# Optimization experiments

Measured on AMD Instinct MI355X. Metric: run time of the kernel, lower is better.

## Reference

```python
import jax, jax.numpy as jnp
import numpy as np

B = 2048
DIMS = [300, 74, 35]
R = 3
ENC = 150
HID = 32
CAT = ENC * R  # 450


def setup_inputs() -> dict:
    key = jax.random.key(0)
    ks = jax.random.split(key, 32)
    d = {}
    for i, dim in enumerate(DIMS):
        d[f"x{i}"] = jax.random.normal(ks[i], (B, 1, dim), dtype=jnp.float32)
    s = 0.05
    for i, dim in enumerate(DIMS):
        d[f"encW{i}"] = jax.random.normal(ks[3 + 2 * i], (ENC, dim), dtype=jnp.float32) * s
        d[f"encb{i}"] = jax.random.normal(ks[4 + 2 * i], (ENC,), dtype=jnp.float32) * s
    d["affw"] = jax.random.normal(ks[10], (R,), dtype=jnp.float32) * s      # Linear(1,1) weight per branch
    d["Ww"] = jax.random.normal(ks[11], (R, HID, 1), dtype=jnp.float32) * s  # Linear(1,32)
    d["Wc"] = jax.random.normal(ks[12], (R, HID, CAT), dtype=jnp.float32) * s  # Linear(450,32)
    d["Wh"] = jax.random.normal(ks[13], (R, 1, HID), dtype=jnp.float32) * s   # Linear(32,1)
    d["clsW1"] = jax.random.normal(ks[14], (128, CAT), dtype=jnp.float32) * s
    d["clsb1"] = jax.random.normal(ks[15], (128,), dtype=jnp.float32) * s
    d["clsW2"] = jax.random.normal(ks[16], (7, 128), dtype=jnp.float32) * s
    d["clsb2"] = jax.random.normal(ks[17], (7,), dtype=jnp.float32) * s
    return d


def reference(x0, x1, x2, encW0, encb0, encW1, encb1, encW2, encb2,
              affw, Ww, Wc, Wh, clsW1, clsb1, clsW2, clsb2):
    xs = [x0, x1, x2]
    encW = [encW0, encW1, encW2]
    encb = [encb0, encb1, encb2]
    # Encode each modality: [B,1,dim_i] -> [B,1,150]
    enc = [jnp.einsum('btd,ed->bte', xs[i], encW[i]) + encb[i] for i in range(R)]
    feat_n = jnp.concatenate(enc, axis=2)            # [B,1,450]
    scale = 1.0 / jnp.sqrt(jnp.float32(feat_n.shape[1]))  # T=1
    att_feats = []
    for i in range(R):
        enc_t = jnp.swapaxes(enc[i], 1, 2)           # [B,150,1]
        t = jnp.swapaxes(feat_n, 1, 2) * affw[i]     # [B,450,1] (Linear(1,1), no bias)
        # outer product attention: [B,150,1] @ [B,1,450] -> [B,150,450]
        att = jnp.tanh(jnp.matmul(enc_t, jnp.swapaxes(t, 1, 2)) * scale)
        a = jnp.einsum('bec,hc->beh', att, Wc[i])    # [B,150,32]
        b = jnp.matmul(enc_t, Ww[i].T)               # [B,150,1]@[1,32] -> [B,150,32]
        H = jax.nn.relu(a + b)
        out_i = jnp.swapaxes(jnp.matmul(H, Wh[i].T), 1, 2) + enc[i]  # [B,1,150]
        att_feats.append(out_i)
    feats = jnp.concatenate(att_feats, axis=2)       # [B,1,450]
    # classifier (dropout is identity in eval mode)
    h = jnp.einsum('btc,kc->btk', feats, clsW1) + clsb1
    return jnp.einsum('btk,ok->bto', h, clsW2) + clsb2
```

## Files before the change

### kernel.cpp

```cpp
#include <hip/hip_runtime.h>
#include <math.h>

#define NJ 4
#define DEG 7
#define X0f 1.1f
#define NB 8
#define NT 768

struct Poly { float c[NJ]; };

typedef float v4f __attribute__((ext_vector_type(4)));

__global__ __launch_bounds__(256) void k_repack(
    const float* __restrict__ Wc, const float* __restrict__ W1,
    const float* __restrict__ eW0, const float* __restrict__ eW1, const float* __restrict__ eW2,
    float* __restrict__ WcT, float* __restrict__ W1T,
    float* __restrict__ Wt0, float* __restrict__ Wt1, float* __restrict__ Wt2) {
    int tid = blockIdx.x * 256 + threadIdx.x;
    int stride = gridDim.x * 256;
    for (int idx = tid; idx < 3 * 464 * 32; idx += stride) {
        int i = idx / (464 * 32); int rem = idx - i * 464 * 32;
        int m = rem >> 5, h = rem & 31;
        float v = 0.f;
        if (m < 456) {
            int seg = m / 152, e = m - seg * 152;
            if (e < 150) v = Wc[((size_t)i * 32 + h) * 450 + seg * 150 + e];
        }
        WcT[idx] = v;
    }
    for (int idx = tid; idx < 456 * 128; idx += stride) {
        int m = idx >> 7, k = idx & 127;
        int seg = m / 152, e = m - seg * 152;
        W1T[idx] = (e < 150) ? W1[k * 450 + seg * 150 + e] : 0.f;
    }
    for (int idx = tid; idx < 304 * 152; idx += stride) {
        int d = idx / 152, e = idx - d * 152;
        Wt0[idx] = (d < 300 && e < 150) ? eW0[e * 300 + d] : 0.f;
    }
    for (int idx = tid; idx < 76 * 152; idx += stride) {
        int d = idx / 152, e = idx - d * 152;
        Wt1[idx] = (d < 74 && e < 150) ? eW1[e * 74 + d] : 0.f;
    }
    for (int idx = tid; idx < 36 * 152; idx += stride) {
        int d = idx / 152, e = idx - d * 152;
        Wt2[idx] = (d < 35 && e < 150) ? eW2[e * 35 + d] : 0.f;
    }
}

__global__ __launch_bounds__(NT, 1) void k_fused(
    const float* __restrict__ x0, const float* __restrict__ x1, const float* __restrict__ x2,
    const float* __restrict__ eb0, const float* __restrict__ eb1, const float* __restrict__ eb2,
    const float* __restrict__ Wt0, const float* __restrict__ Wt1, const float* __restrict__ Wt2,
    const float* __restrict__ WcT,
    const float* __restrict__ affw, const float* __restrict__ Ww, const float* __restrict__ Wh,
    const float* __restrict__ W1T, const float* __restrict__ cb1,
    const float* __restrict__ cW2, const float* __restrict__ cb2,
    float* __restrict__ out, Poly pc) {
#pragma clang fp contract(fast)
    __shared__ __align__(16) float xs[NB * 428];
    __shared__ __align__(16) float featf[NB * 468];
    __shared__ __align__(16) float fof[NB * 468];
    __shared__ __align__(16) float wWs[96], wHs[96];

    int tid = threadIdx.x;
    int b0 = blockIdx.x * NB;

    if (tid < 96) { wWs[tid] = Ww[tid]; wHs[tid] = Wh[tid]; }
    if (tid >= 96 && tid < 192) {
        int q = tid - 96; int b = q / 12, r = q - b * 12;
        featf[b * 468 + 456 + r] = 0.f;
    }
    if (tid >= 192 && tid < 240) {
        int q = tid - 192; int b = q / 6, r = q - b * 6;
        fof[b * 468 + (r >> 1) * 152 + 150 + (r & 1)] = 0.f;
    }
    for (int idx = tid; idx < NB * 75; idx += NT) {
        int b = idx / 75, q = idx - b * 75;
        ((v4f*)(xs + b * 428))[q] = ((const v4f*)(x0 + (size_t)(b0 + b) * 300))[q];
    }
    for (int idx = tid; idx < NB * 74; idx += NT) {
        int b = idx / 74, d = idx - b * 74;
        xs[b * 428 + 304 + d] = x1[(size_t)(b0 + b) * 74 + d];
    }
    for (int idx = tid; idx < NB * 35; idx += NT) {
        int b = idx / 35, d = idx - b * 35;
        xs[b * 428 + 380 + d] = x2[(size_t)(b0 + b) * 35 + d];
    }
    __syncthreads();

    {
        int tasks[2]; int nt = 1;
        tasks[0] = tid;
        if (tid >= 624) { tasks[nt++] = 768 + (767 - tid); }
        for (int q = 0; q < nt; ++q) {
            int task = tasks[q];
            int b = task & 7, m4 = task >> 3;
            int seg = (m4 >= 76) ? 2 : (m4 >= 38) ? 1 : 0;
            int e4 = m4 - seg * 38;
            const float* eb = seg == 0 ? eb0 : seg == 1 ? eb1 : eb2;
            const v4f* Wt4 = (const v4f*)(seg == 0 ? Wt0 : seg == 1 ? Wt1 : Wt2) + e4;
            const float* xb = xs + b * 428 + (seg == 0 ? 0 : seg == 1 ? 304 : 380);
            int DP4 = seg == 0 ? 76 : seg == 1 ? 19 : 9;
            const v4f* xr = (const v4f*)xb;
            int e = e4 * 4;
            v4f acc = { (e < 150) ? eb[e] : 0.f,
                        (e + 1 < 150) ? eb[e + 1] : 0.f,
                        (e + 2 < 150) ? eb[e + 2] : 0.f,
                        (e + 3 < 150) ? eb[e + 3] : 0.f };
            for (int d4 = 0; d4 < DP4; ++d4) {
                v4f x4 = xr[d4];
                v4f w0 = Wt4[(d4 * 4 + 0) * 38];
                v4f w1 = Wt4[(d4 * 4 + 1) * 38];
                v4f w2 = Wt4[(d4 * 4 + 2) * 38];
                v4f w3 = Wt4[(d4 * 4 + 3) * 38];
                acc += x4.x * w0;
                acc += x4.y * w1;
                acc += x4.z * w2;
                acc += x4.w * w3;
            }
            ((v4f*)(featf + b * 468))[m4] = acc;
        }
    }
    __syncthreads();

    {
        int w = tid >> 6;
        int i = w >> 2, wp = w & 3;
        int lane = tid & 63;
        int hq = lane & 7, slice = lane >> 3;
        int slice2 = (lane >> 3) & 3, bh = lane >> 5;
        float aff = affw[i];
        const v4f* Wb4 = (const v4f*)WcT + (size_t)i * 3712 + hq;
        int bA = wp * 2, bB = bA + 1;
        const v4f* frowA = (const v4f*)(featf + bA * 468);
        const v4f* frowB = (const v4f*)(featf + bB * 468);

        v4f accA[NJ], accB[NJ];
        #pragma unroll
        for (int J = 0; J < NJ; ++J) { accA[J] = (v4f)0.f; accB[J] = (v4f)0.f; }
        float mxA = 0.f, mxB = 0.f;

        int m4lo = (slice < 4) ? slice * 15 : 60 + (slice - 4) * 14;
        int m4n  = (slice < 4) ? 15 : 14;
        #pragma unroll 3
        for (int k = 0; k < m4n; ++k) {
            int m4 = m4lo + k;
            v4f fA = frowA[m4];
            v4f fB = frowB[m4];
            const v4f* wp4 = Wb4 + m4 * 32;
            v4f w0 = wp4[0];
            v4f w1 = wp4[8];
            v4f w2 = wp4[16];
            v4f w3 = wp4[24];
            mxA = fmaxf(mxA, fmaxf(fmaxf(fabsf(fA.x), fabsf(fA.y)), fmaxf(fabsf(fA.z), fabsf(fA.w))));
            mxB = fmaxf(mxB, fmaxf(fmaxf(fabsf(fB.x), fabsf(fB.y)), fmaxf(fabsf(fB.z), fabsf(fB.w))));
            {
                float g0 = aff * fA.x, g1 = aff * fA.y, g2 = aff * fA.z, g3 = aff * fA.w;
                float q0 = g0 * g0, q1 = g1 * g1, q2 = g2 * g2, q3 = g3 * g3;
                float p0 = g0, p1 = g1, p2 = g2, p3 = g3;
                accA[0] += p0 * w0; accA[0] += p1 * w1; accA[0] += p2 * w2; accA[0] += p3 * w3;
                #pragma unroll
                for (int J = 1; J < NJ; ++J) {
                    p0 *= q0; p1 *= q1; p2 *= q2; p3 *= q3;
                    accA[J] += p0 * w0; accA[J] += p1 * w1; accA[J] += p2 * w2; accA[J] += p3 * w3;
                }
            }
            {
                float g0 = aff * fB.x, g1 = aff * fB.y, g2 = aff * fB.z, g3 = aff * fB.w;
                float q0 = g0 * g0, q1 = g1 * g1, q2 = g2 * g2, q3 = g3 * g3;
                float p0 = g0, p1 = g1, p2 = g2, p3 = g3;
                accB[0] += p0 * w0; accB[0] += p1 * w1; accB[0] += p2 * w2; accB[0] += p3 * w3;
                #pragma unroll
                for (int J = 1; J < NJ; ++J) {
                    p0 *= q0; p1 *= q1; p2 *= q2; p3 *= q3;
                    accB[J] += p0 * w0; accB[J] += p1 * w1; accB[J] += p2 * w2; accB[J] += p3 * w3;
                }
            }
        }
        #pragma unroll
        for (int J = 0; J < NJ; ++J) {
            float cJ = pc.c[J];
            float vx, vy, vz, vw;
            vx = accA[J].x; vx += __shfl_xor(vx, 8); vx += __shfl_xor(vx, 16); vx += __shfl_xor(vx, 32);
            vy = accA[J].y; vy += __shfl_xor(vy, 8); vy += __shfl_xor(vy, 16); vy += __shfl_xor(vy, 32);
            vz = accA[J].z; vz += __shfl_xor(vz, 8); vz += __shfl_xor(vz, 16); vz += __shfl_xor(vz, 32);
            vw = accA[J].w; vw += __shfl_xor(vw, 8); vw += __shfl_xor(vw, 16); vw += __shfl_xor(vw, 32);
            accA[J] = (v4f){ vx * cJ, vy * cJ, vz * cJ, vw * cJ };
            vx = accB[J].x; vx += __shfl_xor(vx, 8); vx += __shfl_xor(vx, 16); vx += __shfl_xor(vx, 32);
            vy = accB[J].y; vy += __shfl_xor(vy, 8); vy += __shfl_xor(vy, 16); vy += __shfl_xor(vy, 32);
            vz = accB[J].z; vz += __shfl_xor(vz, 8); vz += __shfl_xor(vz, 16); vz += __shfl_xor(vz, 32);
            vw = accB[J].w; vw += __shfl_xor(vw, 8); vw += __shfl_xor(vw, 16); vw += __shfl_xor(vw, 32);
            accB[J] = (v4f){ vx * cJ, vy * cJ, vz * cJ, vw * cJ };
        }
        mxA = fmaxf(mxA, __shfl_xor(mxA, 8));
        mxA = fmaxf(mxA, __shfl_xor(mxA, 16));
        mxA = fmaxf(mxA, __shfl_xor(mxA, 32));
        mxB = fmaxf(mxB, __shfl_xor(mxB, 8));
        mxB = fmaxf(mxB, __shfl_xor(mxB, 16));
        mxB = fmaxf(mxB, __shfl_xor(mxB, 32));

        v4f Ms[NJ];
        #pragma unroll
        for (int J = 0; J < NJ; ++J) Ms[J] = bh ? accB[J] : accA[J];
        float gmax = fabsf(aff) * (bh ? mxB : mxA);
        int b = bA + bh;
        const float* fb = featf + b * 468;
        const v4f* frow = bh ? frowB : frowA;

        v4f wW4 = ((const v4f*)wWs)[i * 8 + hq];
        v4f wH4 = ((const v4f*)wHs)[i * 8 + hq];
        int e4lo = slice2 * 10;
        int e4hi = (slice2 == 3) ? 38 : (e4lo + 10);
        for (int e4 = e4lo; e4 < e4hi; ++e4) {
            v4f s4 = frow[i * 38 + e4];
            float ores[4];
            #pragma unroll
            for (int r = 0; r < 4; ++r) {
                float s = (r == 0) ? s4.x : (r == 1) ? s4.y : (r == 2) ? s4.z : s4.w;
                v4f a4;
                if (fabsf(s) * gmax <= X0f) {
                    float s2 = s * s, p = s;
                    a4 = Ms[0] * p;
                    #pragma unroll
                    for (int J = 1; J < NJ; ++J) { p *= s2; a4 += p * Ms[J]; }
                } else {
                    a4 = (v4f)0.f;
                    for (int c = 0; c < 456; ++c) {
                        float t = tanhf(s * aff * fb[c]);
                        a4 += t * Wb4[c * 8];
                    }
                }
                v4f hv = s * wW4 + a4;
                hv = __builtin_elementwise_max(hv, (v4f)0.f);
                v4f dv = hv * wH4;
                float csum = dv.x + dv.y + dv.z + dv.w;
                csum += __shfl_xor(csum, 1);
                csum += __shfl_xor(csum, 2);
                csum += __shfl_xor(csum, 4);
                ores[r] = csum + s;
            }
            if (hq == 0)
                ((v4f*)(fof + b * 468))[i * 38 + e4] = (v4f){ ores[0], ores[1], ores[2], ores[3] };
        }
    }
    __syncthreads();

    {
        int cs = tid >> 8;
        int rr = tid & 255;
        int b = rr & 7, k4 = rr >> 3;
        const v4f* W14 = (const v4f*)W1T + k4;
        const v4f* fr = (const v4f*)(fof + b * 468);
        v4f a = (v4f)0.f;
        int c4lo = cs * 38;
        for (int c4 = c4lo; c4 < c4lo + 38; ++c4) {
            v4f fv = fr[c4];
            v4f w0 = W14[(c4 * 4 + 0) * 32];
            v4f w1 = W14[(c4 * 4 + 1) * 32];
            v4f w2 = W14[(c4 * 4 + 2) * 32];
            v4f w3 = W14[(c4 * 4 + 3) * 32];
            a += fv.x * w0;
            a += fv.y * w1;
            a += fv.z * w2;
            a += fv.w * w3;
        }
        ((v4f*)xs)[(cs * 8 + b) * 33 + k4] = a;
    }
    __syncthreads();
    if (tid < 256) {
        int b = tid >> 5, k4 = tid & 31;
        const v4f* hp4 = (const v4f*)xs;
        v4f v  = hp4[(0 * 8 + b) * 33 + k4];
        v4f v1 = hp4[(1 * 8 + b) * 33 + k4];
        v4f v2 = hp4[(2 * 8 + b) * 33 + k4];
        v4f bias = ((const v4f*)cb1)[k4];
        v = v + v1 + v2 + bias;
        ((v4f*)(featf + b * 468))[k4] = v;
    }
    __syncthreads();
    if (tid < NB * 7) {
        int b = tid / 7, o = tid - (tid / 7) * 7;
        const v4f* hb = (const v4f*)(featf + b * 468);
        const v4f* w2 = (const v4f*)(cW2 + o * 128);
        v4f a4 = (v4f)0.f;
        #pragma unroll 8
        for (int k4 = 0; k4 < 32; ++k4) a4 += hb[k4] * w2[k4];
        out[(size_t)(b0 + b) * 7 + o] = cb2[o] + a4.x + a4.y + a4.z + a4.w;
    }
}

static void make_poly(float* cf) {
    const double a = 1.1;
    const int NQ = 128;
    const double PI = 3.14159265358979323846;
    double b[DEG + 1];
    for (int k = 0; k <= DEG; ++k) b[k] = 0.0;
    for (int m = 0; m < NQ; ++m) {
        double th = PI * (m + 0.5) / NQ;
        double f = tanh(a * cos(th));
        for (int k = 1; k <= DEG; k += 2)
            b[k] += (2.0 / NQ) * f * cos(k * th);
    }
    double Tp[DEG + 1], Tc[DEG + 1], Tn[DEG + 1], mono[DEG + 1];
    for (int j = 0; j <= DEG; ++j) { Tp[j] = 0; Tc[j] = 0; mono[j] = 0; }
    Tp[0] = 1.0;
    Tc[1] = 1.0;
    for (int j = 0; j <= DEG; ++j) mono[j] += b[1] * Tc[j];
    for (int k = 2; k <= DEG; ++k) {
        for (int j = 0; j <= DEG; ++j) Tn[j] = -Tp[j];
        for (int j = 1; j <= DEG; ++j) Tn[j] += 2.0 * Tc[j - 1];
        for (int j = 0; j <= DEG; ++j) { Tp[j] = Tc[j]; Tc[j] = Tn[j]; }
        if (k & 1) for (int j = 0; j <= DEG; ++j) mono[j] += b[k] * Tc[j];
    }
    for (int J = 0; J < NJ; ++J) {
        int j = 2 * J + 1;
        cf[J] = (float)(mono[j] / pow(a, (double)j));
    }
}

extern "C" void kernel_launch(void* const* d_in, const int* in_sizes, int n_in,
                              void* d_out, int out_size, void* d_ws, size_t ws_size,
                              hipStream_t stream) {
    (void)in_sizes; (void)n_in; (void)out_size; (void)ws_size;
    const float* x0    = (const float*)d_in[0];
    const float* x1    = (const float*)d_in[1];
    const float* x2    = (const float*)d_in[2];
    const float* eW0   = (const float*)d_in[3];
    const float* eb0   = (const float*)d_in[4];
    const float* eW1   = (const float*)d_in[5];
    const float* eb1   = (const float*)d_in[6];
    const float* eW2   = (const float*)d_in[7];
    const float* eb2   = (const float*)d_in[8];
    const float* affw  = (const float*)d_in[9];
    const float* Ww    = (const float*)d_in[10];
    const float* Wc    = (const float*)d_in[11];
    const float* Wh    = (const float*)d_in[12];
    const float* cW1   = (const float*)d_in[13];
    const float* cb1   = (const float*)d_in[14];
    const float* cW2   = (const float*)d_in[15];
    const float* cb2   = (const float*)d_in[16];

    float* ws    = (float*)d_ws;
    float* wsWcT = ws;
    float* wsW1T = ws + 44544;
    float* wsWt0 = ws + 102912;
    float* wsWt1 = ws + 149120;
    float* wsWt2 = ws + 160672;

    Poly pc;
    make_poly(pc.c);

    k_repack<<<dim3(96), dim3(256), 0, stream>>>(Wc, cW1, eW0, eW1, eW2,
                                                 wsWcT, wsW1T, wsWt0, wsWt1, wsWt2);
    k_fused<<<dim3(256), dim3(NT), 0, stream>>>(x0, x1, x2, eb0, eb1, eb2,
                                                wsWt0, wsWt1, wsWt2, wsWcT,
                                                affw, Ww, Wh, wsW1T, cb1, cW2, cb2,
                                                (float*)d_out, pc);
}
```

Baseline: 66.04 us.

## Raise block to 1024 threads and split polynomial moment pass across all waves

The block size grows to 1024 threads. The encoder stage now gives one task per thread, dropping the two-task tail. The polynomial moment accumulation is split into its own phase: all 16 waves each handle three (branch, batch, half) units, store partial moments and abs-max values to shared memory, and a later phase of 12 waves combines them and runs the tanh/relu evaluation. The classifier reduction is also spread over four slices instead of three. This aims to raise parallelism and shorten the critical path, at the cost of an extra barrier, shared-memory round trips and higher register pressure at 1024 threads.

```diff
diff --git a/kernel.cpp b/kernel.cpp
--- a/kernel.cpp
+++ b/kernel.cpp
@@ -5,7 +5,7 @@
 #define DEG 7
 #define X0f 1.1f
 #define NB 8
-#define NT 768
+#define NT 1024
 
 struct Poly { float c[NJ]; };
 
@@ -57,13 +57,17 @@
     const float* __restrict__ cW2, const float* __restrict__ cb2,
     float* __restrict__ out, Poly pc) {
 #pragma clang fp contract(fast)
-    __shared__ __align__(16) float xs[NB * 428];
+    __shared__ __align__(16) float R[6144];
     __shared__ __align__(16) float featf[NB * 468];
     __shared__ __align__(16) float fof[NB * 468];
     __shared__ __align__(16) float wWs[96], wHs[96];
+    __shared__ float mxs[48];
 
     int tid = threadIdx.x;
     int b0 = blockIdx.x * NB;
+    float* xs = R;
+    v4f* Mp4 = (v4f*)R;
+    v4f* clsP4 = (v4f*)R;
 
     if (tid < 96) { wWs[tid] = Ww[tid]; wHs[tid] = Wh[tid]; }
     if (tid >= 96 && tid < 192) {
@@ -88,159 +92,137 @@
     }
     __syncthreads();
 
+    if (tid < 912) {
+        int b = tid & 7, m4 = tid >> 3;
+        int seg = (m4 >= 76) ? 2 : (m4 >= 38) ? 1 : 0;
+        int e4 = m4 - seg * 38;
+        const float* eb = seg == 0 ? eb0 : seg == 1 ? eb1 : eb2;
+        const v4f* Wt4 = (const v4f*)(seg == 0 ? Wt0 : seg == 1 ? Wt1 : Wt2) + e4;
+        const float* xb = xs + b * 428 + (seg == 0 ? 0 : seg == 1 ? 304 : 380);
+        int DP4 = seg == 0 ? 76 : seg == 1 ? 19 : 9;
+        const v4f* xr = (const v4f*)xb;
+        int e = e4 * 4;
+        v4f acc = { (e < 150) ? eb[e] : 0.f,
+                    (e + 1 < 150) ? eb[e + 1] : 0.f,
+                    (e + 2 < 150) ? eb[e + 2] : 0.f,
+                    (e + 3 < 150) ? eb[e + 3] : 0.f };
+        for (int d4 = 0; d4 < DP4; ++d4) {
+            v4f x4 = xr[d4];
+            v4f w0 = Wt4[(d4 * 4 + 0) * 38];
+            v4f w1 = Wt4[(d4 * 4 + 1) * 38];
+            v4f w2 = Wt4[(d4 * 4 + 2) * 38];
+            v4f w3 = Wt4[(d4 * 4 + 3) * 38];
+            acc += x4.x * w0;
+            acc += x4.y * w1;
+            acc += x4.z * w2;
+            acc += x4.w * w3;
+        }
+        ((v4f*)(featf + b * 468))[m4] = acc;
+    }
+    __syncthreads();
+
     {
-        int tasks[2]; int nt = 1;
-        tasks[0] = tid;
-        if (tid >= 624) { tasks[nt++] = 768 + (767 - tid); }
-        for (int q = 0; q < nt; ++q) {
-            int task = tasks[q];
-            int b = task & 7, m4 = task >> 3;
-            int seg = (m4 >= 76) ? 2 : (m4 >= 38) ? 1 : 0;
-            int e4 = m4 - seg * 38;
-            const float* eb = seg == 0 ? eb0 : seg == 1 ? eb1 : eb2;
-            const v4f* Wt4 = (const v4f*)(seg == 0 ? Wt0 : seg == 1 ? Wt1 : Wt2) + e4;
-            const float* xb = xs + b * 428 + (seg == 0 ? 0 : seg == 1 ? 304 : 380);
-            int DP4 = seg == 0 ? 76 : seg == 1 ? 19 : 9;
-            const v4f* xr = (const v4f*)xb;
-            int e = e4 * 4;
-            v4f acc = { (e < 150) ? eb[e] : 0.f,
-                        (e + 1 < 150) ? eb[e + 1] : 0.f,
-                        (e + 2 < 150) ? eb[e + 2] : 0.f,
-                        (e + 3 < 150) ? eb[e + 3] : 0.f };
-            for (int d4 = 0; d4 < DP4; ++d4) {
-                v4f x4 = xr[d4];
-                v4f w0 = Wt4[(d4 * 4 + 0) * 38];
-                v4f w1 = Wt4[(d4 * 4 + 1) * 38];
-                v4f w2 = Wt4[(d4 * 4 + 2) * 38];
-                v4f w3 = Wt4[(d4 * 4 + 3) * 38];
-                acc += x4.x * w0;
-                acc += x4.y * w1;
-                acc += x4.z * w2;
-                acc += x4.w * w3;
+        int w = tid >> 6, lane = tid & 63;
+        int hq = lane & 7, slice = (lane >> 3) & 7;
+        #pragma unroll
+        for (int q = 0; q < 3; ++q) {
+            int h = w * 3 + q;
+            int u = h >> 1, ch = h & 1;
+            int i = u >> 3, b = u & 7;
+            float aff = affw[i];
+            const v4f* Wb4 = (const v4f*)WcT + (size_t)i * 3712 + hq;
+            const float* fb = featf + b * 468;
+            int clo = ch * 228 + ((slice < 4) ? slice * 29 : 116 + (slice - 4) * 28);
+            int cn = (slice < 4) ? 29 : 28;
+            v4f acc[NJ];
+            #pragma unroll
+            for (int J = 0; J < NJ; ++J) acc[J] = (v4f)0.f;
+            float mx = 0.f;
+            #pragma unroll 4
+            for (int k = 0; k < cn; ++k) {
+                int c = clo + k;
+                float f = fb[c];
+                v4f wv = Wb4[(size_t)c * 8];
+                mx = fmaxf(mx, fabsf(f));
+                float g = aff * f, g2 = g * g;
+                float p = g;
+                acc[0] += p * wv;
+                #pragma unroll
+                for (int J = 1; J < NJ; ++J) { p *= g2; acc[J] += p * wv; }
             }
-            ((v4f*)(featf + b * 468))[m4] = acc;
+            #pragma unroll
+            for (int J = 0; J < NJ; ++J) {
+                float cJ = pc.c[J];
+                float vx = acc[J].x; vx += __shfl_xor(vx, 8); vx += __shfl_xor(vx, 16); vx += __shfl_xor(vx, 32);
+                float vy = acc[J].y; vy += __shfl_xor(vy, 8); vy += __shfl_xor(vy, 16); vy += __shfl_xor(vy, 32);
+                float vz = acc[J].z; vz += __shfl_xor(vz, 8); vz += __shfl_xor(vz, 16); vz += __shfl_xor(vz, 32);
+                float vw = acc[J].w; vw += __shfl_xor(vw, 8); vw += __shfl_xor(vw, 16); vw += __shfl_xor(vw, 32);
+                acc[J] = (v4f){ vx * cJ, vy * cJ, vz * cJ, vw * cJ };
+            }
+            mx = fmaxf(mx, __shfl_xor(mx, 8));
+            mx = fmaxf(mx, __shfl_xor(mx, 16));
+            mx = fmaxf(mx, __shfl_xor(mx, 32));
+            if (slice == 0) {
+                #pragma unroll
+                for (int J = 0; J < NJ; ++J) Mp4[(h * 8 + hq) * 4 + J] = acc[J];
+                if (hq == 0) mxs[h] = mx;
+            }
         }
     }
     __syncthreads();
 
     {
-        int w = tid >> 6;
-        int i = w >> 2, wp = w & 3;
-        int lane = tid & 63;
-        int hq = lane & 7, slice = lane >> 3;
-        int slice2 = (lane >> 3) & 3, bh = lane >> 5;
-        float aff = affw[i];
-        const v4f* Wb4 = (const v4f*)WcT + (size_t)i * 3712 + hq;
-        int bA = wp * 2, bB = bA + 1;
-        const v4f* frowA = (const v4f*)(featf + bA * 468);
-        const v4f* frowB = (const v4f*)(featf + bB * 468);
-
-        v4f accA[NJ], accB[NJ];
-        #pragma unroll
-        for (int J = 0; J < NJ; ++J) { accA[J] = (v4f)0.f; accB[J] = (v4f)0.f; }
-        float mxA = 0.f, mxB = 0.f;
-
-        int m4lo = (slice < 4) ? slice * 15 : 60 + (slice - 4) * 14;
-        int m4n  = (slice < 4) ? 15 : 14;
-        #pragma unroll 3
-        for (int k = 0; k < m4n; ++k) {
-            int m4 = m4lo + k;
-            v4f fA = frowA[m4];
-            v4f fB = frowB[m4];
-            const v4f* wp4 = Wb4 + m4 * 32;
-            v4f w0 = wp4[0];
-            v4f w1 = wp4[8];
-            v4f w2 = wp4[16];
-            v4f w3 = wp4[24];
-            mxA = fmaxf(mxA, fmaxf(fmaxf(fabsf(fA.x), fabsf(fA.y)), fmaxf(fabsf(fA.z), fabsf(fA.w))));
-            mxB = fmaxf(mxB, fmaxf(fmaxf(fabsf(fB.x), fabsf(fB.y)), fmaxf(fabsf(fB.z), fabsf(fB.w))));
-            {
-                float g0 = aff * fA.x, g1 = aff * fA.y, g2 = aff * fA.z, g3 = aff * fA.w;
-                float q0 = g0 * g0, q1 = g1 * g1, q2 = g2 * g2, q3 = g3 * g3;
-                float p0 = g0, p1 = g1, p2 = g2, p3 = g3;
-                accA[0] += p0 * w0; accA[0] += p1 * w1; accA[0] += p2 * w2; accA[0] += p3 * w3;
+        int w = tid >> 6, lane = tid & 63;
+        if (w < 12) {
+            int i = w >> 2, wp = w & 3;
+            int hq = lane & 7, slice2 = (lane >> 3) & 3, bh = lane >> 5;
+            int b = wp * 2 + bh;
+            int u = i * 8 + b;
+            float aff = affw[i];
+            const v4f* Wb4 = (const v4f*)WcT + (size_t)i * 3712;
+            const float* fb = featf + b * 468;
+            const v4f* frow = (const v4f*)fb;
+            v4f Ms[NJ];
+            #pragma unroll
+            for (int J = 0; J < NJ; ++J)
+                Ms[J] = Mp4[((2 * u) * 8 + hq) * 4 + J] + Mp4[((2 * u + 1) * 8 + hq) * 4 + J];
+            float gmax = fabsf(aff) * fmaxf(mxs[2 * u], mxs[2 * u + 1]);
+
+            v4f wW4 = ((const v4f*)wWs)[i * 8 + hq];
+            v4f wH4 = ((const v4f*)wHs)[i * 8 + hq];
+            int e4lo = slice2 * 10;
+            int e4hi = (slice2 == 3) ? 38 : (e4lo + 10);
+            for (int e4 = e4lo; e4 < e4hi; ++e4) {
+                v4f s4 = frow[i * 38 + e4];
+                float ores[4];
                 #pragma unroll
-                for (int J = 1; J < NJ; ++J) {
-                    p0 *= q0; p1 *= q1; p2 *= q2; p3 *= q3;
-                    accA[J] += p0 * w0; accA[J] += p1 * w1; accA[J] += p2 * w2; accA[J] += p3 * w3;
+                for (int r = 0; r < 4; ++r) {
+                    float s = (r == 0) ? s4.x : (r == 1) ? s4.y : (r == 2) ? s4.z : s4.w;
+                    v4f a4;
+                    if (fabsf(s) * gmax <= X0f) {
+                        float s2 = s * s, p = s;
+                        a4 = Ms[0] * p;
+                        #pragma unroll
+                        for (int J = 1; J < NJ; ++J) { p *= s2; a4 += p * Ms[J]; }
+                    } else {
+                        a4 = (v4f)0.f;
+                        for (int c = 0; c < 456; ++c) {
+                            float t = tanhf(s * aff * fb[c]);
+                            a4 += t * Wb4[(size_t)c * 8 + hq];
+                        }
+                    }
+                    v4f hv = s * wW4 + a4;
+                    hv = __builtin_elementwise_max(hv, (v4f)0.f);
+                    v4f dv = hv * wH4;
+                    float csum = dv.x + dv.y + dv.z + dv.w;
+                    csum += __shfl_xor(csum, 1);
+                    csum += __shfl_xor(csum, 2);
+                    csum += __shfl_xor(csum, 4);
+                    ores[r] = csum + s;
                 }
+                if (hq == 0)
+                    ((v4f*)(fof + b * 468))[i * 38 + e4] = (v4f){ ores[0], ores[1], ores[2], ores[3] };
             }
-            {
-                float g0 = aff * fB.x, g1 = aff * fB.y, g2 = aff * fB.z, g3 = aff * fB.w;
-                float q0 = g0 * g0, q1 = g1 * g1, q2 = g2 * g2, q3 = g3 * g3;
-                float p0 = g0, p1 = g1, p2 = g2, p3 = g3;
-                accB[0] += p0 * w0; accB[0] += p1 * w1; accB[0] += p2 * w2; accB[0] += p3 * w3;
-                #pragma unroll
-                for (int J = 1; J < NJ; ++J) {
-                    p0 *= q0; p1 *= q1; p2 *= q2; p3 *= q3;
-                    accB[J] += p0 * w0; accB[J] += p1 * w1; accB[J] += p2 * w2; accB[J] += p3 * w3;
-                }
-            }
-        }
-        #pragma unroll
-        for (int J = 0; J < NJ; ++J) {
-            float cJ = pc.c[J];
-            float vx, vy, vz, vw;
-            vx = accA[J].x; vx += __shfl_xor(vx, 8); vx += __shfl_xor(vx, 16); vx += __shfl_xor(vx, 32);
-            vy = accA[J].y; vy += __shfl_xor(vy, 8); vy += __shfl_xor(vy, 16); vy += __shfl_xor(vy, 32);
-            vz = accA[J].z; vz += __shfl_xor(vz, 8); vz += __shfl_xor(vz, 16); vz += __shfl_xor(vz, 32);
-            vw = accA[J].w; vw += __shfl_xor(vw, 8); vw += __shfl_xor(vw, 16); vw += __shfl_xor(vw, 32);
-            accA[J] = (v4f){ vx * cJ, vy * cJ, vz * cJ, vw * cJ };
-            vx = accB[J].x; vx += __shfl_xor(vx, 8); vx += __shfl_xor(vx, 16); vx += __shfl_xor(vx, 32);
-            vy = accB[J].y; vy += __shfl_xor(vy, 8); vy += __shfl_xor(vy, 16); vy += __shfl_xor(vy, 32);
-            vz = accB[J].z; vz += __shfl_xor(vz, 8); vz += __shfl_xor(vz, 16); vz += __shfl_xor(vz, 32);
-            vw = accB[J].w; vw += __shfl_xor(vw, 8); vw += __shfl_xor(vw, 16); vw += __shfl_xor(vw, 32);
-            accB[J] = (v4f){ vx * cJ, vy * cJ, vz * cJ, vw * cJ };
-        }
-        mxA = fmaxf(mxA, __shfl_xor(mxA, 8));
-        mxA = fmaxf(mxA, __shfl_xor(mxA, 16));
-        mxA = fmaxf(mxA, __shfl_xor(mxA, 32));
-        mxB = fmaxf(mxB, __shfl_xor(mxB, 8));
-        mxB = fmaxf(mxB, __shfl_xor(mxB, 16));
-        mxB = fmaxf(mxB, __shfl_xor(mxB, 32));
-
-        v4f Ms[NJ];
-        #pragma unroll
-        for (int J = 0; J < NJ; ++J) Ms[J] = bh ? accB[J] : accA[J];
-        float gmax = fabsf(aff) * (bh ? mxB : mxA);
-        int b = bA + bh;
-        const float* fb = featf + b * 468;
-        const v4f* frow = bh ? frowB : frowA;
-
-        v4f wW4 = ((const v4f*)wWs)[i * 8 + hq];
-        v4f wH4 = ((const v4f*)wHs)[i * 8 + hq];
-        int e4lo = slice2 * 10;
-        int e4hi = (slice2 == 3) ? 38 : (e4lo + 10);
-        for (int e4 = e4lo; e4 < e4hi; ++e4) {
-            v4f s4 = frow[i * 38 + e4];
-            float ores[4];
-            #pragma unroll
-            for (int r = 0; r < 4; ++r) {
-                float s = (r == 0) ? s4.x : (r == 1) ? s4.y : (r == 2) ? s4.z : s4.w;
-                v4f a4;
-                if (fabsf(s) * gmax <= X0f) {
-                    float s2 = s * s, p = s;
-                    a4 = Ms[0] * p;
-                    #pragma unroll
-                    for (int J = 1; J < NJ; ++J) { p *= s2; a4 += p * Ms[J]; }
-                } else {
-                    a4 = (v4f)0.f;
-                    for (int c = 0; c < 456; ++c) {
-                        float t = tanhf(s * aff * fb[c]);
-                        a4 += t * Wb4[c * 8];
-                    }
-                }
-                v4f hv = s * wW4 + a4;
-                hv = __builtin_elementwise_max(hv, (v4f)0.f);
-                v4f dv = hv * wH4;
-                float csum = dv.x + dv.y + dv.z + dv.w;
-                csum += __shfl_xor(csum, 1);
-                csum += __shfl_xor(csum, 2);
-                csum += __shfl_xor(csum, 4);
-                ores[r] = csum + s;
-            }
-            if (hq == 0)
-                ((v4f*)(fof + b * 468))[i * 38 + e4] = (v4f){ ores[0], ores[1], ores[2], ores[3] };
         }
     }
     __syncthreads();
@@ -252,8 +234,10 @@
         const v4f* W14 = (const v4f*)W1T + k4;
         const v4f* fr = (const v4f*)(fof + b * 468);
         v4f a = (v4f)0.f;
-        int c4lo = cs * 38;
-        for (int c4 = c4lo; c4 < c4lo + 38; ++c4) {
+        int c4lo = (cs < 2) ? cs * 29 : 58 + (cs - 2) * 28;
+        int c4n  = (cs < 2) ? 29 : 28;
+        for (int k = 0; k < c4n; ++k) {
+            int c4 = c4lo + k;
             v4f fv = fr[c4];
             v4f w0 = W14[(c4 * 4 + 0) * 32];
             v4f w1 = W14[(c4 * 4 + 1) * 32];
@@ -264,17 +248,14 @@
             a += fv.z * w2;
             a += fv.w * w3;
         }
-        ((v4f*)xs)[(cs * 8 + b) * 33 + k4] = a;
+        clsP4[(cs * 8 + b) * 32 + k4] = a;
     }
     __syncthreads();
     if (tid < 256) {
         int b = tid >> 5, k4 = tid & 31;
-        const v4f* hp4 = (const v4f*)xs;
-        v4f v  = hp4[(0 * 8 + b) * 33 + k4];
-        v4f v1 = hp4[(1 * 8 + b) * 33 + k4];
-        v4f v2 = hp4[(2 * 8 + b) * 33 + k4];
-        v4f bias = ((const v4f*)cb1)[k4];
-        v = v + v1 + v2 + bias;
+        v4f v = ((const v4f*)cb1)[k4];
+        #pragma unroll
+        for (int cs = 0; cs < 4; ++cs) v += clsP4[(cs * 8 + b) * 32 + k4];
         ((v4f*)(featf + b * 468))[k4] = v;
     }
     __syncthreads();
```

After: 67.49 us. 2.2% more time.

## Split fused kernel into encoder, attention and classifier kernels via global workspace

Applied to the files above, without the earlier changes.

Replaces the single 256-block fused kernel (8 rows per 768-thread block, staged through shared memory) with three kernels: encoder, attention and classifier. They exchange intermediates through global workspace buffers, and the attention kernel runs 3072 small 64-thread blocks. The aim is more parallelism and occupancy across the GPU's CUs. The cost is two extra launches, global-memory round trips for the encoded features and attention outputs, and more redundant weight loads per block.

```diff
diff --git a/kernel.cpp b/kernel.cpp
--- a/kernel.cpp
+++ b/kernel.cpp
@@ -4,8 +4,7 @@
 #define NJ 4
 #define DEG 7
 #define X0f 1.1f
-#define NB 8
-#define NT 768
+#define ESTR 464
 
 struct Poly { float c[NJ]; };
 
@@ -47,213 +46,202 @@
     }
 }
 
-__global__ __launch_bounds__(NT, 1) void k_fused(
+__global__ __launch_bounds__(256) void k_enc(
     const float* __restrict__ x0, const float* __restrict__ x1, const float* __restrict__ x2,
     const float* __restrict__ eb0, const float* __restrict__ eb1, const float* __restrict__ eb2,
     const float* __restrict__ Wt0, const float* __restrict__ Wt1, const float* __restrict__ Wt2,
-    const float* __restrict__ WcT,
-    const float* __restrict__ affw, const float* __restrict__ Ww, const float* __restrict__ Wh,
-    const float* __restrict__ W1T, const float* __restrict__ cb1,
-    const float* __restrict__ cW2, const float* __restrict__ cb2,
-    float* __restrict__ out, Poly pc) {
+    float* __restrict__ wsEnc) {
 #pragma clang fp contract(fast)
-    __shared__ __align__(16) float xs[NB * 428];
-    __shared__ __align__(16) float featf[NB * 468];
-    __shared__ __align__(16) float fof[NB * 468];
-    __shared__ __align__(16) float wWs[96], wHs[96];
-
     int tid = threadIdx.x;
-    int b0 = blockIdx.x * NB;
-
-    if (tid < 96) { wWs[tid] = Ww[tid]; wHs[tid] = Wh[tid]; }
-    if (tid >= 96 && tid < 192) {
-        int q = tid - 96; int b = q / 12, r = q - b * 12;
-        featf[b * 468 + 456 + r] = 0.f;
-    }
-    if (tid >= 192 && tid < 240) {
-        int q = tid - 192; int b = q / 6, r = q - b * 6;
-        fof[b * 468 + (r >> 1) * 152 + 150 + (r & 1)] = 0.f;
-    }
-    for (int idx = tid; idx < NB * 75; idx += NT) {
-        int b = idx / 75, q = idx - b * 75;
-        ((v4f*)(xs + b * 428))[q] = ((const v4f*)(x0 + (size_t)(b0 + b) * 300))[q];
-    }
-    for (int idx = tid; idx < NB * 74; idx += NT) {
-        int b = idx / 74, d = idx - b * 74;
-        xs[b * 428 + 304 + d] = x1[(size_t)(b0 + b) * 74 + d];
-    }
-    for (int idx = tid; idx < NB * 35; idx += NT) {
-        int b = idx / 35, d = idx - b * 35;
-        xs[b * 428 + 380 + d] = x2[(size_t)(b0 + b) * 35 + d];
-    }
-    __syncthreads();
-
-    {
-        int tasks[2]; int nt = 1;
-        tasks[0] = tid;
-        if (tid >= 624) { tasks[nt++] = 768 + (767 - tid); }
-        for (int q = 0; q < nt; ++q) {
-            int task = tasks[q];
-            int b = task & 7, m4 = task >> 3;
-            int seg = (m4 >= 76) ? 2 : (m4 >= 38) ? 1 : 0;
-            int e4 = m4 - seg * 38;
-            const float* eb = seg == 0 ? eb0 : seg == 1 ? eb1 : eb2;
-            const v4f* Wt4 = (const v4f*)(seg == 0 ? Wt0 : seg == 1 ? Wt1 : Wt2) + e4;
-            const float* xb = xs + b * 428 + (seg == 0 ? 0 : seg == 1 ? 304 : 380);
-            int DP4 = seg == 0 ? 76 : seg == 1 ? 19 : 9;
-            const v4f* xr = (const v4f*)xb;
-            int e = e4 * 4;
-            v4f acc = { (e < 150) ? eb[e] : 0.f,
-                        (e + 1 < 150) ? eb[e + 1] : 0.f,
-                        (e + 2 < 150) ? eb[e + 2] : 0.f,
-                        (e + 3 < 150) ? eb[e + 3] : 0.f };
-            for (int d4 = 0; d4 < DP4; ++d4) {
+    int b0 = blockIdx.x * 4;
+    if (tid < 32) {
+        int b = tid >> 3, j = tid & 7;
+        wsEnc[(size_t)(b0 + b) * ESTR + 456 + j] = 0.f;
+    }
+    for (int task = tid; task < 456; task += 256) {
+        int b = task & 3, m4 = task >> 2;
+        int row = b0 + b;
+        int seg = (m4 >= 76) ? 2 : (m4 >= 38) ? 1 : 0;
+        int e4 = m4 - seg * 38;
+        int e = e4 * 4;
+        const float* eb = seg == 0 ? eb0 : seg == 1 ? eb1 : eb2;
+        v4f acc = { (e < 150) ? eb[e] : 0.f,
+                    (e + 1 < 150) ? eb[e + 1] : 0.f,
+                    (e + 2 < 150) ? eb[e + 2] : 0.f,
+                    (e + 3 < 150) ? eb[e + 3] : 0.f };
+        if (seg == 0) {
+            const v4f* W4 = (const v4f*)Wt0 + e4;
+            const v4f* xr = (const v4f*)(x0 + (size_t)row * 300);
+            for (int d4 = 0; d4 < 75; ++d4) {
                 v4f x4 = xr[d4];
-                v4f w0 = Wt4[(d4 * 4 + 0) * 38];
-                v4f w1 = Wt4[(d4 * 4 + 1) * 38];
-                v4f w2 = Wt4[(d4 * 4 + 2) * 38];
-                v4f w3 = Wt4[(d4 * 4 + 3) * 38];
+                v4f w0 = W4[(d4 * 4 + 0) * 38];
+                v4f w1 = W4[(d4 * 4 + 1) * 38];
+                v4f w2 = W4[(d4 * 4 + 2) * 38];
+                v4f w3 = W4[(d4 * 4 + 3) * 38];
                 acc += x4.x * w0;
                 acc += x4.y * w1;
                 acc += x4.z * w2;
                 acc += x4.w * w3;
             }
-            ((v4f*)(featf + b * 468))[m4] = acc;
-        }
-    }
-    __syncthreads();
-
-    {
-        int w = tid >> 6;
-        int i = w >> 2, wp = w & 3;
-        int lane = tid & 63;
-        int hq = lane & 7, slice = lane >> 3;
-        int slice2 = (lane >> 3) & 3, bh = lane >> 5;
-        float aff = affw[i];
-        const v4f* Wb4 = (const v4f*)WcT + (size_t)i * 3712 + hq;
-        int bA = wp * 2, bB = bA + 1;
-        const v4f* frowA = (const v4f*)(featf + bA * 468);
-        const v4f* frowB = (const v4f*)(featf + bB * 468);
-
-        v4f accA[NJ], accB[NJ];
+        } else if (seg == 1) {
+            const v4f* W4 = (const v4f*)Wt1 + e4;
+            const float* xb = x1 + (size_t)row * 74;
+            #pragma unroll 2
+            for (int d = 0; d < 74; ++d) acc += xb[d] * W4[d * 38];
+        } else {
+            const v4f* W4 = (const v4f*)Wt2 + e4;
+            const float* xb = x2 + (size_t)row * 35;
+            #pragma unroll 5
+            for (int d = 0; d < 35; ++d) acc += xb[d] * W4[d * 38];
+        }
+        ((v4f*)(wsEnc + (size_t)row * ESTR))[m4] = acc;
+    }
+}
+
+__global__ __launch_bounds__(64) void k_attn(
+    const float* __restrict__ wsEnc,
+    const float* __restrict__ WcT,
+    const float* __restrict__ affw, const float* __restrict__ Ww, const float* __restrict__ Wh,
+    float* __restrict__ fof, Poly pc) {
+#pragma clang fp contract(fast)
+    int lane = threadIdx.x;
+    int i = blockIdx.y;
+    int bA = blockIdx.x * 2, bB = bA + 1;
+    int hq = lane & 7, slice = lane >> 3;
+    int slice2 = (lane >> 3) & 3, bh = lane >> 5;
+    float aff = affw[i];
+    const v4f* Wb4 = (const v4f*)WcT + (size_t)i * 3712 + hq;
+    const v4f* frowA = (const v4f*)(wsEnc + (size_t)bA * ESTR);
+    const v4f* frowB = (const v4f*)(wsEnc + (size_t)bB * ESTR);
+
+    v4f accA[NJ], accB[NJ];
+    #pragma unroll
+    for (int J = 0; J < NJ; ++J) { accA[J] = (v4f)0.f; accB[J] = (v4f)0.f; }
+    float mxA = 0.f, mxB = 0.f;
+
+    int m4lo = (slice < 4) ? slice * 15 : 60 + (slice - 4) * 14;
+    int m4n  = (slice < 4) ? 15 : 14;
+    #pragma unroll 3
+    for (int k = 0; k < m4n; ++k) {
+        int m4 = m4lo + k;
+        v4f fA = frowA[m4];
+        v4f fB = frowB[m4];
+        const v4f* wp4 = Wb4 + m4 * 32;
+        v4f w0 = wp4[0];
+        v4f w1 = wp4[8];
+        v4f w2 = wp4[16];
+        v4f w3 = wp4[24];
+        mxA = fmaxf(mxA, fmaxf(fmaxf(fabsf(fA.x), fabsf(fA.y)), fmaxf(fabsf(fA.z), fabsf(fA.w))));
+        mxB = fmaxf(mxB, fmaxf(fmaxf(fabsf(fB.x), fabsf(fB.y)), fmaxf(fabsf(fB.z), fabsf(fB.w))));
+        {
+            float g0 = aff * fA.x, g1 = aff * fA.y, g2 = aff * fA.z, g3 = aff * fA.w;
+            float q0 = g0 * g0, q1 = g1 * g1, q2 = g2 * g2, q3 = g3 * g3;
+            float p0 = g0, p1 = g1, p2 = g2, p3 = g3;
+            accA[0] += p0 * w0; accA[0] += p1 * w1; accA[0] += p2 * w2; accA[0] += p3 * w3;
+            #pragma unroll
+            for (int J = 1; J < NJ; ++J) {
+                p0 *= q0; p1 *= q1; p2 *= q2; p3 *= q3;
+                accA[J] += p0 * w0; accA[J] += p1 * w1; accA[J] += p2 * w2; accA[J] += p3 * w3;
+            }
+        }
+        {
+            float g0 = aff * fB.x, g1 = aff * fB.y, g2 = aff * fB.z, g3 = aff * fB.w;
+            float q0 = g0 * g0, q1 = g1 * g1, q2 = g2 * g2, q3 = g3 * g3;
+            float p0 = g0, p1 = g1, p2 = g2, p3 = g3;
+            accB[0] += p0 * w0; accB[0] += p1 * w1; accB[0] += p2 * w2; accB[0] += p3 * w3;
+            #pragma unroll
+            for (int J = 1; J < NJ; ++J) {
+                p0 *= q0; p1 *= q1; p2 *= q2; p3 *= q3;
+                accB[J] += p0 * w0; accB[J] += p1 * w1; accB[J] += p2 * w2; accB[J] += p3 * w3;
+            }
+        }
+    }
+    #pragma unroll
+    for (int J = 0; J < NJ; ++J) {
+        float cJ = pc.c[J];
+        float vx, vy, vz, vw;
+        vx = accA[J].x; vx += __shfl_xor(vx, 8); vx += __shfl_xor(vx, 16); vx += __shfl_xor(vx, 32);
+        vy = accA[J].y; vy += __shfl_xor(vy, 8); vy += __shfl_xor(vy, 16); vy += __shfl_xor(vy, 32);
+        vz = accA[J].z; vz += __shfl_xor(vz, 8); vz += __shfl_xor(vz, 16); vz += __shfl_xor(vz, 32);
+        vw = accA[J].w; vw += __shfl_xor(vw, 8); vw += __shfl_xor(vw, 16); vw += __shfl_xor(vw, 32);
+        accA[J] = (v4f){ vx * cJ, vy * cJ, vz * cJ, vw * cJ };
+        vx = accB[J].x; vx += __shfl_xor(vx, 8); vx += __shfl_xor(vx, 16); vx += __shfl_xor(vx, 32);
+        vy = accB[J].y; vy += __shfl_xor(vy, 8); vy += __shfl_xor(vy, 16); vy += __shfl_xor(vy, 32);
+        vz = accB[J].z; vz += __shfl_xor(vz, 8); vz += __shfl_xor(vz, 16); vz += __shfl_xor(vz, 32);
+        vw = accB[J].w; vw += __shfl_xor(vw, 8); vw += __shfl_xor(vw, 16); vw += __shfl_xor(vw, 32);
+        accB[J] = (v4f){ vx * cJ, vy * cJ, vz * cJ, vw * cJ };
+    }
+    mxA = fmaxf(mxA, __shfl_xor(mxA, 8));
+    mxA = fmaxf(mxA, __shfl_xor(mxA, 16));
+    mxA = fmaxf(mxA, __shfl_xor(mxA, 32));
+    mxB = fmaxf(mxB, __shfl_xor(mxB, 8));
+    mxB = fmaxf(mxB, __shfl_xor(mxB, 16));
+    mxB = fmaxf(mxB, __shfl_xor(mxB, 32));
+
+    v4f Ms[NJ];
+    #pragma unroll
+    for (int J = 0; J < NJ; ++J) Ms[J] = bh ? accB[J] : accA[J];
+    float gmax = fabsf(aff) * (bh ? mxB : mxA);
+    int b = bA + bh;
+    const float* fb = wsEnc + (size_t)b * ESTR;
+    const v4f* frow = bh ? frowB : frowA;
+
+    v4f wW4 = ((const v4f*)(Ww + i * 32))[hq];
+    v4f wH4 = ((const v4f*)(Wh + i * 32))[hq];
+    int e4lo = slice2 * 10;
+    int e4hi = (slice2 == 3) ? 38 : (e4lo + 10);
+    for (int e4 = e4lo; e4 < e4hi; ++e4) {
+        v4f s4 = frow[i * 38 + e4];
+        float ores[4];
         #pragma unroll
-        for (int J = 0; J < NJ; ++J) { accA[J] = (v4f)0.f; accB[J] = (v4f)0.f; }
-        float mxA = 0.f, mxB = 0.f;
-
-        int m4lo = (slice < 4) ? slice * 15 : 60 + (slice - 4) * 14;
-        int m4n  = (slice < 4) ? 15 : 14;
-        #pragma unroll 3
-        for (int k = 0; k < m4n; ++k) {
-            int m4 = m4lo + k;
-            v4f fA = frowA[m4];
-            v4f fB = frowB[m4];
-            const v4f* wp4 = Wb4 + m4 * 32;
-            v4f w0 = wp4[0];
-            v4f w1 = wp4[8];
-            v4f w2 = wp4[16];
-            v4f w3 = wp4[24];
-            mxA = fmaxf(mxA, fmaxf(fmaxf(fabsf(fA.x), fabsf(fA.y)), fmaxf(fabsf(fA.z), fabsf(fA.w))));
-            mxB = fmaxf(mxB, fmaxf(fmaxf(fabsf(fB.x), fabsf(fB.y)), fmaxf(fabsf(fB.z), fabsf(fB.w))));
-            {
-                float g0 = aff * fA.x, g1 = aff * fA.y, g2 = aff * fA.z, g3 = aff * fA.w;
-                float q0 = g0 * g0, q1 = g1 * g1, q2 = g2 * g2, q3 = g3 * g3;
-                float p0 = g0, p1 = g1, p2 = g2, p3 = g3;
-                accA[0] += p0 * w0; accA[0] += p1 * w1; accA[0] += p2 * w2; accA[0] += p3 * w3;
+        for (int r = 0; r < 4; ++r) {
+            float s = (r == 0) ? s4.x : (r == 1) ? s4.y : (r == 2) ? s4.z : s4.w;
+            v4f a4;
+            if (fabsf(s) * gmax <= X0f) {
+                float s2 = s * s, p = s;
+                a4 = Ms[0] * p;
                 #pragma unroll
-                for (int J = 1; J < NJ; ++J) {
-                    p0 *= q0; p1 *= q1; p2 *= q2; p3 *= q3;
-                    accA[J] += p0 * w0; accA[J] += p1 * w1; accA[J] += p2 * w2; accA[J] += p3 * w3;
+                for (int J = 1; J < NJ; ++J) { p *= s2; a4 += p * Ms[J]; }
+            } else {
+                a4 = (v4f)0.f;
+                for (int c = 0; c < 456; ++c) {
+                    float t = tanhf(s * aff * fb[c]);
+                    a4 += t * Wb4[(size_t)c * 8];
                 }
             }
-            {
-                float g0 = aff * fB.x, g1 = aff * fB.y, g2 = aff * fB.z, g3 = aff * fB.w;
-                float q0 = g0 * g0, q1 = g1 * g1, q2 = g2 * g2, q3 = g3 * g3;
-                float p0 = g0, p1 = g1, p2 = g2, p3 = g3;
-                accB[0] += p0 * w0; accB[0] += p1 * w1; accB[0] += p2 * w2; accB[0] += p3 * w3;
-                #pragma unroll
-                for (int J = 1; J < NJ; ++J) {
-                    p0 *= q0; p1 *= q1; p2 *= q2; p3 *= q3;
-                    accB[J] += p0 * w0; accB[J] += p1 * w1; accB[J] += p2 * w2; accB[J] += p3 * w3;
-                }
-            }
-        }
-        #pragma unroll
-        for (int J = 0; J < NJ; ++J) {
-            float cJ = pc.c[J];
-            float vx, vy, vz, vw;
-            vx = accA[J].x; vx += __shfl_xor(vx, 8); vx += __shfl_xor(vx, 16); vx += __shfl_xor(vx, 32);
-            vy = accA[J].y; vy += __shfl_xor(vy, 8); vy += __shfl_xor(vy, 16); vy += __shfl_xor(vy, 32);
-            vz = accA[J].z; vz += __shfl_xor(vz, 8); vz += __shfl_xor(vz, 16); vz += __shfl_xor(vz, 32);
-            vw = accA[J].w; vw += __shfl_xor(vw, 8); vw += __shfl_xor(vw, 16); vw += __shfl_xor(vw, 32);
-            accA[J] = (v4f){ vx * cJ, vy * cJ, vz * cJ, vw * cJ };
-            vx = accB[J].x; vx += __shfl_xor(vx, 8); vx += __shfl_xor(vx, 16); vx += __shfl_xor(vx, 32);
-            vy = accB[J].y; vy += __shfl_xor(vy, 8); vy += __shfl_xor(vy, 16); vy += __shfl_xor(vy, 32);
-            vz = accB[J].z; vz += __shfl_xor(vz, 8); vz += __shfl_xor(vz, 16); vz += __shfl_xor(vz, 32);
-            vw = accB[J].w; vw += __shfl_xor(vw, 8); vw += __shfl_xor(vw, 16); vw += __shfl_xor(vw, 32);
-            accB[J] = (v4f){ vx * cJ, vy * cJ, vz * cJ, vw * cJ };
-        }
-        mxA = fmaxf(mxA, __shfl_xor(mxA, 8));
-        mxA = fmaxf(mxA, __shfl_xor(mxA, 16));
-        mxA = fmaxf(mxA, __shfl_xor(mxA, 32));
-        mxB = fmaxf(mxB, __shfl_xor(mxB, 8));
-        mxB = fmaxf(mxB, __shfl_xor(mxB, 16));
-        mxB = fmaxf(mxB, __shfl_xor(mxB, 32));
-
-        v4f Ms[NJ];
-        #pragma unroll
-        for (int J = 0; J < NJ; ++J) Ms[J] = bh ? accB[J] : accA[J];
-        float gmax = fabsf(aff) * (bh ? mxB : mxA);
-        int b = bA + bh;
-        const float* fb = featf + b * 468;
-        const v4f* frow = bh ? frowB : frowA;
-
-        v4f wW4 = ((const v4f*)wWs)[i * 8 + hq];
-        v4f wH4 = ((const v4f*)wHs)[i * 8 + hq];
-        int e4lo = slice2 * 10;
-        int e4hi = (slice2 == 3) ? 38 : (e4lo + 10);
-        for (int e4 = e4lo; e4 < e4hi; ++e4) {
-            v4f s4 = frow[i * 38 + e4];
-            float ores[4];
-            #pragma unroll
-            for (int r = 0; r < 4; ++r) {
-                float s = (r == 0) ? s4.x : (r == 1) ? s4.y : (r == 2) ? s4.z : s4.w;
-                v4f a4;
-                if (fabsf(s) * gmax <= X0f) {
-                    float s2 = s * s, p = s;
-                    a4 = Ms[0] * p;
-                    #pragma unroll
-                    for (int J = 1; J < NJ; ++J) { p *= s2; a4 += p * Ms[J]; }
-                } else {
-                    a4 = (v4f)0.f;
-                    for (int c = 0; c < 456; ++c) {
-                        float t = tanhf(s * aff * fb[c]);
-                        a4 += t * Wb4[c * 8];
-                    }
-                }
-                v4f hv = s * wW4 + a4;
-                hv = __builtin_elementwise_max(hv, (v4f)0.f);
-                v4f dv = hv * wH4;
-                float csum = dv.x + dv.y + dv.z + dv.w;
-                csum += __shfl_xor(csum, 1);
-                csum += __shfl_xor(csum, 2);
-                csum += __shfl_xor(csum, 4);
-                ores[r] = csum + s;
-            }
-            if (hq == 0)
-                ((v4f*)(fof + b * 468))[i * 38 + e4] = (v4f){ ores[0], ores[1], ores[2], ores[3] };
-        }
-    }
-    __syncthreads();
-
+            v4f hv = s * wW4 + a4;
+            hv = __builtin_elementwise_max(hv, (v4f)0.f);
+            v4f dv = hv * wH4;
+            float csum = dv.x + dv.y + dv.z + dv.w;
+            csum += __shfl_xor(csum, 1);
+            csum += __shfl_xor(csum, 2);
+            csum += __shfl_xor(csum, 4);
+            ores[r] = csum + s;
+        }
+        if (hq == 0)
+            ((v4f*)(fof + (size_t)b * 456))[i * 38 + e4] = (v4f){ ores[0], ores[1], ores[2], ores[3] };
+    }
+}
+
+__global__ __launch_bounds__(256) void k_cls(
+    const float* __restrict__ fof,
+    const float* __restrict__ W1T, const float* __restrict__ cb1,
+    const float* __restrict__ cW2, const float* __restrict__ cb2,
+    float* __restrict__ out) {
+#pragma clang fp contract(fast)
+    __shared__ __align__(16) float clsP[2 * 4 * 32 * 4];
+    __shared__ __align__(16) float hs[4][132];
+    int tid = threadIdx.x;
+    int b0 = blockIdx.x * 4;
     {
-        int cs = tid >> 8;
-        int rr = tid & 255;
-        int b = rr & 7, k4 = rr >> 3;
-        const v4f* W14 = (const v4f*)W1T + k4;
-        const v4f* fr = (const v4f*)(fof + b * 468);
+        int ch = tid >> 7;
+        int rr = tid & 127;
+        int b = rr & 3, kq = rr >> 2;
+        const v4f* W14 = (const v4f*)W1T + kq;
+        const v4f* fr = (const v4f*)(fof + (size_t)(b0 + b) * 456);
         v4f a = (v4f)0.f;
-        int c4lo = cs * 38;
-        for (int c4 = c4lo; c4 < c4lo + 38; ++c4) {
+        int c4lo = ch * 57;
+        for (int c4 = c4lo; c4 < c4lo + 57; ++c4) {
             v4f fv = fr[c4];
             v4f w0 = W14[(c4 * 4 + 0) * 32];
             v4f w1 = W14[(c4 * 4 + 1) * 32];
@@ -264,23 +252,20 @@
             a += fv.z * w2;
             a += fv.w * w3;
         }
-        ((v4f*)xs)[(cs * 8 + b) * 33 + k4] = a;
+        ((v4f*)clsP)[(ch * 4 + b) * 32 + kq] = a;
     }
     __syncthreads();
-    if (tid < 256) {
-        int b = tid >> 5, k4 = tid & 31;
-        const v4f* hp4 = (const v4f*)xs;
-        v4f v  = hp4[(0 * 8 + b) * 33 + k4];
-        v4f v1 = hp4[(1 * 8 + b) * 33 + k4];
-        v4f v2 = hp4[(2 * 8 + b) * 33 + k4];
-        v4f bias = ((const v4f*)cb1)[k4];
-        v = v + v1 + v2 + bias;
-        ((v4f*)(featf + b * 468))[k4] = v;
+    if (tid < 128) {
+        int b = tid >> 5, kq = tid & 31;
+        v4f v = ((const v4f*)cb1)[kq];
+        v += ((const v4f*)clsP)[(0 * 4 + b) * 32 + kq];
+        v += ((const v4f*)clsP)[(1 * 4 + b) * 32 + kq];
+        *((v4f*)&hs[b][kq * 4]) = v;
     }
     __syncthreads();
-    if (tid < NB * 7) {
+    if (tid < 28) {
         int b = tid / 7, o = tid - (tid / 7) * 7;
-        const v4f* hb = (const v4f*)(featf + b * 468);
+        const v4f* hb = (const v4f*)&hs[b][0];
         const v4f* w2 = (const v4f*)(cW2 + o * 128);
         v4f a4 = (v4f)0.f;
         #pragma unroll 8
@@ -346,14 +331,16 @@
     float* wsWt0 = ws + 102912;
     float* wsWt1 = ws + 149120;
     float* wsWt2 = ws + 160672;
+    float* wsEnc = ws + 166144;
+    float* wsFof = ws + 1116416;
 
     Poly pc;
     make_poly(pc.c);
 
     k_repack<<<dim3(96), dim3(256), 0, stream>>>(Wc, cW1, eW0, eW1, eW2,
                                                  wsWcT, wsW1T, wsWt0, wsWt1, wsWt2);
-    k_fused<<<dim3(256), dim3(NT), 0, stream>>>(x0, x1, x2, eb0, eb1, eb2,
-                                                wsWt0, wsWt1, wsWt2, wsWcT,
-                                                affw, Ww, Wh, wsW1T, cb1, cW2, cb2,
-                                                (float*)d_out, pc);
-}
+    k_enc<<<dim3(512), dim3(256), 0, stream>>>(x0, x1, x2, eb0, eb1, eb2,
+                                               wsWt0, wsWt1, wsWt2, wsEnc);
+    k_attn<<<dim3(1024, 3), dim3(64), 0, stream>>>(wsEnc, wsWcT, affw, Ww, Wh, wsFof, pc);
+    k_cls<<<dim3(512), dim3(256), 0, stream>>>(wsFof, wsW1T, cb1, cW2, cb2, (float*)d_out);
+}
```

Result: slower. 95.45 us (+44.5%).
